# Kernel optimization log

Hardware: AMD Instinct MI355X
Metric: run time of the kernel (lower is better)

## Reference

```python
import jax, jax.numpy as jnp
import numpy as np

B = 8192      # batch size
D = 512       # feature dim == num_classes (centers is [C, C] in the original)
C = 512       # num_classes
MARGIN = 1.0


def setup_inputs() -> dict:
    key = jax.random.key(0)
    k1, k2, k3 = jax.random.split(key, 3)
    inputs = jax.random.normal(k1, (B, D), dtype=jnp.float32)
    targets = jax.random.randint(k2, (B,), 0, C)
    centers = jax.random.normal(k3, (C, D), dtype=jnp.float32)  # learned param
    return {"inputs": inputs, "targets": targets, "centers": centers}


def reference(inputs, targets, centers):
    # centers_batch[j] = centers[targets[j]]  (gather rows)
    cb = centers[targets]                                   # [B, D]
    # dist[i, j] = || inputs[i] - cb[j] ||_2, computed via the expanded form
    # (||a||^2 + ||b||^2 - 2 a.b) so we never materialize a [B, B, D] tensor.
    sq = ((inputs * inputs).sum(-1)[:, None]
          + (cb * cb).sum(-1)[None, :]
          - 2.0 * (inputs @ cb.T))                          # [B, B]
    dist = jnp.sqrt(jnp.clip(sq, 1e-12))                    # clamp(min=1e-12).sqrt()

    # mask[i, j] = (targets[i] == targets[j]); note original indexes dist[i][mask[i]]
    mask = targets[:, None] == targets[None, :]             # [B, B] bool
    dist_ap = jnp.max(jnp.where(mask, dist, -jnp.inf), axis=1)   # hardest positive per row
    dist_an = jnp.min(jnp.where(mask, jnp.inf, dist), axis=1)    # hardest negative per row

    # MarginRankingLoss(margin)(dist_an, dist_ap, y=1) = mean(relu(dist_ap - dist_an + margin))
    loss = jnp.mean(jnp.maximum(0.0, dist_ap - dist_an + MARGIN))
    prec = jnp.mean((dist_an > dist_ap).astype(jnp.float32))
    return loss, prec
```

## Files before the change

kernel.cpp:

```cpp
#include <hip/hip_runtime.h>
#include <hip/hip_bf16.h>

#define NB 8192
#define ND 512
#define NC 512
#define MARGIN_F 1.0f
#define BIGF 3.0e38f

typedef __attribute__((ext_vector_type(8))) short bf16x8;
typedef __attribute__((ext_vector_type(4))) float f32x4;

__device__ __forceinline__ unsigned fkey(float f) {
    unsigned u = __float_as_uint(f);
    unsigned mask = (u & 0x80000000u) ? 0xFFFFFFFFu : 0x80000000u;
    return u ^ mask;
}
__device__ __forceinline__ float finv(unsigned k) {
    unsigned mask = (k & 0x80000000u) ? 0x80000000u : 0xFFFFFFFFu;
    return __uint_as_float(k ^ mask);
}
__device__ __forceinline__ unsigned short f2bf(float f) {
    __hip_bfloat16 h = __float2bfloat16(f);
    return __builtin_bit_cast(unsigned short, h);
}

#define GLOAD_LDS16(g, l)                                                    \
    __builtin_amdgcn_global_load_lds(                                        \
        (const __attribute__((address_space(1))) void*)(g),                  \
        (__attribute__((address_space(3))) void*)(l), 16, 0, 0)

__global__ __launch_bounds__(256) void k0_prep(
    const float* __restrict__ inputs, const int* __restrict__ targets,
    const float* __restrict__ centers,
    unsigned short* __restrict__ inB, unsigned short* __restrict__ cenB,
    float* __restrict__ rsq, float* __restrict__ csq,
    unsigned* __restrict__ counts, unsigned* __restrict__ negmin)
{
    const int bid = blockIdx.x;
    const int tid = threadIdx.x;

    if (bid == 2176) {
        __shared__ unsigned hist[NC];
        for (int i = tid; i < NC; i += 256) hist[i] = 0u;
        __syncthreads();
        for (int i = tid; i < NB; i += 256) atomicAdd(&hist[targets[i]], 1u);
        __syncthreads();
        for (int i = tid; i < NC; i += 256) counts[i] = hist[i];
        return;
    }

    const int wave = tid >> 6, lane = tid & 63;
    const float* src;
    unsigned short* dst;
    float* sqdst;
    int row;
    bool is_input = (bid < 2048);
    if (is_input) {
        row   = bid * 4 + wave;
        src   = inputs + (size_t)row * ND;
        dst   = inB + (size_t)row * ND;
        sqdst = rsq + row;
    } else {
        row   = (bid - 2048) * 4 + wave;
        src   = centers + (size_t)row * ND;
        dst   = cenB + (size_t)row * ND;
        sqdst = csq + row;
    }

    float4 v1 = ((const float4*)src)[lane];
    float4 v2 = ((const float4*)src)[lane + 64];
    float s = v1.x*v1.x + v1.y*v1.y + v1.z*v1.z + v1.w*v1.w
            + v2.x*v2.x + v2.y*v2.y + v2.z*v2.z + v2.w*v2.w;

    ushort4 o1, o2;
    o1.x = f2bf(v1.x); o1.y = f2bf(v1.y); o1.z = f2bf(v1.z); o1.w = f2bf(v1.w);
    o2.x = f2bf(v2.x); o2.y = f2bf(v2.y); o2.z = f2bf(v2.z); o2.w = f2bf(v2.w);
    ((ushort4*)dst)[lane]      = o1;
    ((ushort4*)dst)[lane + 64] = o2;

    #pragma unroll
    for (int off = 32; off > 0; off >>= 1) s += __shfl_down(s, off);
    if (lane == 0) {
        *sqdst = s;
        if (is_input) negmin[row] = 0xFFFFFFFFu;
    }
}

__global__ __launch_bounds__(256) void k2_mfma(
    const unsigned short* __restrict__ Ain, const unsigned short* __restrict__ cenB,
    const int* __restrict__ targets, const unsigned* __restrict__ counts,
    const float* __restrict__ csq,
    unsigned* __restrict__ negmin, float* __restrict__ apval)
{
    __shared__ __align__(16) unsigned short As[16 * 512];
    __shared__ __align__(16) unsigned short Bs[8 * 512];
    __shared__ int      tgtL[128];
    __shared__ float    csqL[64];
    __shared__ unsigned ldsmin[128];

    const int tid  = threadIdx.x;
    const int w    = tid >> 6;
    const int lane = tid & 63;
    const int wm   = w >> 1;
    const int wn   = w & 1;
    const int ln   = lane & 15;
    const int kc8  = (lane >> 4) * 8;

    const int bid   = blockIdx.x;
    const int rbase = (bid & 63) * 128;
    const int cbase = (bid >> 6) * 64;

    if (tid < 128) { tgtL[tid] = targets[rbase + tid]; ldsmin[tid] = 0xFFFFFFFFu; }
    if (tid < 64) {
        const int c = cbase + tid;
        csqL[tid] = (counts[c] > 0u) ? csq[c] : BIGF;
    }

    const unsigned short* gAp[4];
    unsigned short*       lAp[4];
    #pragma unroll
    for (int t = 0; t < 4; ++t) {
        const int cid = 4 * w + t;
        const int rg = cid >> 1, kh = cid & 1;
        gAp[t] = Ain + (size_t)(rbase + rg * 16 + ln) * ND + kh * 32 + kc8;
        lAp[t] = &As[cid * 512];
    }
    const unsigned short* gBp[2];
    unsigned short*       lBp[2];
    #pragma unroll
    for (int t = 0; t < 2; ++t) {
        const int cid = 2 * w + t;
        gBp[t] = cenB + (size_t)(cbase + w * 16 + ln) * ND + t * 32 + kc8;
        lBp[t] = &Bs[cid * 512];
    }

    f32x4 acc[4][2] = {};

    for (int kb = 0; kb < ND; kb += 64) {
        __syncthreads();
        #pragma unroll
        for (int t = 0; t < 4; ++t) GLOAD_LDS16(gAp[t] + kb, lAp[t]);
        #pragma unroll
        for (int t = 0; t < 2; ++t) GLOAD_LDS16(gBp[t] + kb, lBp[t]);
        __syncthreads();

        #pragma unroll
        for (int ks = 0; ks < 2; ++ks) {
            bf16x8 a[4], b[2];
            #pragma unroll
            for (int i = 0; i < 4; ++i)
                a[i] = *(const bf16x8*)&As[((wm * 4 + i) * 2 + ks) * 512 + lane * 8];
            #pragma unroll
            for (int j = 0; j < 2; ++j)
                b[j] = *(const bf16x8*)&Bs[((wn * 2 + j) * 2 + ks) * 512 + lane * 8];
            #pragma unroll
            for (int i = 0; i < 4; ++i)
                #pragma unroll
                for (int j = 0; j < 2; ++j)
                    acc[i][j] = __builtin_amdgcn_mfma_f32_16x16x32_bf16(a[i], b[j], acc[i][j], 0, 0, 0);
        }
    }

    const int qd = lane >> 4;
    #pragma unroll
    for (int i = 0; i < 4; ++i) {
        #pragma unroll
        for (int r = 0; r < 4; ++r) {
            const int rlocal = wm * 64 + i * 16 + qd * 4 + r;
            const int grow   = rbase + rlocal;
            const int tr     = tgtL[rlocal];
            float m = BIGF;
            #pragma unroll
            for (int j = 0; j < 2; ++j) {
                const int clocal = wn * 32 + j * 16 + ln;
                const float val = csqL[clocal] - 2.0f * acc[i][j][r];
                if (cbase + clocal == tr) {
                    apval[grow] = val;
                } else {
                    m = fminf(m, val);
                }
            }
            #pragma unroll
            for (int off = 1; off < 16; off <<= 1)
                m = fminf(m, __shfl_xor(m, off));
            if (ln == 0) atomicMin(&ldsmin[rlocal], fkey(m));
        }
    }
    __syncthreads();
    if (tid < 128) {
        unsigned v = ldsmin[tid];
        if (v != 0xFFFFFFFFu) atomicMin(&negmin[rbase + tid], v);
    }
}

__global__ __launch_bounds__(1024) void k3_final(
    const float* __restrict__ rsq, const unsigned* __restrict__ negmin,
    const float* __restrict__ apval, float* __restrict__ out)
{
    __shared__ float sl[1024];
    __shared__ float sp[1024];
    const int tid = threadIdx.x;
    float a = 0.0f, p = 0.0f;
    for (int r = tid; r < NB; r += 1024) {
        float s  = rsq[r];
        float an = sqrtf(fmaxf(s + finv(negmin[r]), 1e-12f));
        float ap = sqrtf(fmaxf(s + apval[r], 1e-12f));
        a += fmaxf(0.0f, ap - an + MARGIN_F);
        p += (an > ap) ? 1.0f : 0.0f;
    }
    sl[tid] = a; sp[tid] = p;
    __syncthreads();
    #pragma unroll
    for (int s = 512; s > 0; s >>= 1) {
        if (tid < s) { sl[tid] += sl[tid + s]; sp[tid] += sp[tid + s]; }
        __syncthreads();
    }
    if (tid == 0) {
        out[0] = sl[0] / (float)NB;
        out[1] = sp[0] / (float)NB;
    }
}

extern "C" void kernel_launch(void* const* d_in, const int* in_sizes, int n_in,
                              void* d_out, int out_size, void* d_ws, size_t ws_size,
                              hipStream_t stream) {
    const float* inputs  = (const float*)d_in[0];
    const int*   targets = (const int*)d_in[1];
    const float* centers = (const float*)d_in[2];
    float* out = (float*)d_out;

    char* wp = (char*)d_ws;
    unsigned short* inB    = (unsigned short*)(wp);
    unsigned short* cenB   = (unsigned short*)(wp + 8388608);
    float*          rsq    = (float*)(wp + 8912896);
    float*          csqv   = (float*)(wp + 8945664);
    unsigned*       counts = (unsigned*)(wp + 8947712);
    unsigned*       negmin = (unsigned*)(wp + 8949760);
    float*          apval  = (float*)(wp + 8982528);

    k0_prep<<<2177, 256, 0, stream>>>(inputs, targets, centers,
                                      inB, cenB, rsq, csqv, counts, negmin);
    k2_mfma<<<512, 256, 0, stream>>>(inB, cenB, targets, counts, csqv,
                                     negmin, apval);
    k3_final<<<1, 1024, 0, stream>>>(rsq, negmin, apval, out);
}
```

Baseline: 97.63 us.

## Halve row tile to double grid and replace atomic min with per-tile partials

```diff
diff --git a/kernel.cpp b/kernel.cpp
--- a/kernel.cpp
+++ b/kernel.cpp
@@ -4,6 +4,7 @@
 #define NB 8192
 #define ND 512
 #define NC 512
+#define NCT 8
 #define MARGIN_F 1.0f
 #define BIGF 3.0e38f
 
@@ -34,7 +35,7 @@
     const float* __restrict__ centers,
     unsigned short* __restrict__ inB, unsigned short* __restrict__ cenB,
     float* __restrict__ rsq, float* __restrict__ csq,
-    unsigned* __restrict__ counts, unsigned* __restrict__ negmin)
+    unsigned* __restrict__ counts)
 {
     const int bid = blockIdx.x;
     const int tid = threadIdx.x;
@@ -80,23 +81,20 @@
 
     #pragma unroll
     for (int off = 32; off > 0; off >>= 1) s += __shfl_down(s, off);
-    if (lane == 0) {
-        *sqdst = s;
-        if (is_input) negmin[row] = 0xFFFFFFFFu;
-    }
+    if (lane == 0) *sqdst = s;
 }
 
 __global__ __launch_bounds__(256) void k2_mfma(
     const unsigned short* __restrict__ Ain, const unsigned short* __restrict__ cenB,
     const int* __restrict__ targets, const unsigned* __restrict__ counts,
     const float* __restrict__ csq,
-    unsigned* __restrict__ negmin, float* __restrict__ apval)
+    float* __restrict__ partmin, float* __restrict__ apval)
 {
-    __shared__ __align__(16) unsigned short As[16 * 512];
+    __shared__ __align__(16) unsigned short As[8 * 512];
     __shared__ __align__(16) unsigned short Bs[8 * 512];
-    __shared__ int      tgtL[128];
+    __shared__ int      tgtL[64];
     __shared__ float    csqL[64];
-    __shared__ unsigned ldsmin[128];
+    __shared__ unsigned ldsmin[64];
 
     const int tid  = threadIdx.x;
     const int w    = tid >> 6;
@@ -104,69 +102,65 @@
     const int wm   = w >> 1;
     const int wn   = w & 1;
     const int ln   = lane & 15;
-    const int kc8  = (lane >> 4) * 8;
+    const int qd   = lane >> 4;
 
     const int bid   = blockIdx.x;
-    const int rbase = (bid & 63) * 128;
-    const int cbase = (bid >> 6) * 64;
-
-    if (tid < 128) { tgtL[tid] = targets[rbase + tid]; ldsmin[tid] = 0xFFFFFFFFu; }
+    const int rbase = (bid & 127) * 64;
+    const int ct    = bid >> 7;
+    const int cbase = ct * 64;
+
     if (tid < 64) {
+        tgtL[tid]   = targets[rbase + tid];
         const int c = cbase + tid;
-        csqL[tid] = (counts[c] > 0u) ? csq[c] : BIGF;
-    }
-
-    const unsigned short* gAp[4];
-    unsigned short*       lAp[4];
-    #pragma unroll
-    for (int t = 0; t < 4; ++t) {
-        const int cid = 4 * w + t;
-        const int rg = cid >> 1, kh = cid & 1;
-        gAp[t] = Ain + (size_t)(rbase + rg * 16 + ln) * ND + kh * 32 + kc8;
-        lAp[t] = &As[cid * 512];
-    }
+        csqL[tid]   = (counts[c] > 0u) ? csq[c] : BIGF;
+        ldsmin[tid] = 0xFFFFFFFFu;
+    }
+
+    const unsigned short* gAp[2];
     const unsigned short* gBp[2];
-    unsigned short*       lBp[2];
+    unsigned short *lAp[2], *lBp[2];
     #pragma unroll
     for (int t = 0; t < 2; ++t) {
         const int cid = 2 * w + t;
-        gBp[t] = cenB + (size_t)(cbase + w * 16 + ln) * ND + t * 32 + kc8;
+        gAp[t] = Ain  + (size_t)(rbase + w * 16 + ln) * ND + t * 32 + qd * 8;
+        gBp[t] = cenB + (size_t)(cbase + w * 16 + ln) * ND + t * 32 + qd * 8;
+        lAp[t] = &As[cid * 512];
         lBp[t] = &Bs[cid * 512];
     }
 
-    f32x4 acc[4][2] = {};
+    f32x4 acc[2][2] = {};
 
     for (int kb = 0; kb < ND; kb += 64) {
         __syncthreads();
         #pragma unroll
-        for (int t = 0; t < 4; ++t) GLOAD_LDS16(gAp[t] + kb, lAp[t]);
-        #pragma unroll
-        for (int t = 0; t < 2; ++t) GLOAD_LDS16(gBp[t] + kb, lBp[t]);
+        for (int t = 0; t < 2; ++t) {
+            GLOAD_LDS16(gAp[t] + kb, lAp[t]);
+            GLOAD_LDS16(gBp[t] + kb, lBp[t]);
+        }
         __syncthreads();
 
         #pragma unroll
         for (int ks = 0; ks < 2; ++ks) {
-            bf16x8 a[4], b[2];
-            #pragma unroll
-            for (int i = 0; i < 4; ++i)
-                a[i] = *(const bf16x8*)&As[((wm * 4 + i) * 2 + ks) * 512 + lane * 8];
+            bf16x8 a[2], b[2];
+            #pragma unroll
+            for (int i = 0; i < 2; ++i)
+                a[i] = *(const bf16x8*)&As[((wm * 2 + i) * 2 + ks) * 512 + lane * 8];
             #pragma unroll
             for (int j = 0; j < 2; ++j)
                 b[j] = *(const bf16x8*)&Bs[((wn * 2 + j) * 2 + ks) * 512 + lane * 8];
             #pragma unroll
-            for (int i = 0; i < 4; ++i)
+            for (int i = 0; i < 2; ++i)
                 #pragma unroll
                 for (int j = 0; j < 2; ++j)
                     acc[i][j] = __builtin_amdgcn_mfma_f32_16x16x32_bf16(a[i], b[j], acc[i][j], 0, 0, 0);
         }
     }
 
-    const int qd = lane >> 4;
-    #pragma unroll
-    for (int i = 0; i < 4; ++i) {
+    #pragma unroll
+    for (int i = 0; i < 2; ++i) {
         #pragma unroll
         for (int r = 0; r < 4; ++r) {
-            const int rlocal = wm * 64 + i * 16 + qd * 4 + r;
+            const int rlocal = wm * 32 + i * 16 + qd * 4 + r;
             const int grow   = rbase + rlocal;
             const int tr     = tgtL[rlocal];
             float m = BIGF;
@@ -187,23 +181,27 @@
         }
     }
     __syncthreads();
-    if (tid < 128) {
-        unsigned v = ldsmin[tid];
-        if (v != 0xFFFFFFFFu) atomicMin(&negmin[rbase + tid], v);
-    }
+    if (tid < 64)
+        partmin[(size_t)(rbase + tid) * NCT + ct] = finv(ldsmin[tid]);
 }
 
 __global__ __launch_bounds__(1024) void k3_final(
-    const float* __restrict__ rsq, const unsigned* __restrict__ negmin,
+    const float* __restrict__ rsq, const float* __restrict__ partmin,
     const float* __restrict__ apval, float* __restrict__ out)
 {
     __shared__ float sl[1024];
     __shared__ float sp[1024];
     const int tid = threadIdx.x;
     float a = 0.0f, p = 0.0f;
-    for (int r = tid; r < NB; r += 1024) {
+    #pragma unroll
+    for (int it = 0; it < NB / 1024; ++it) {
+        const int r = it * 1024 + tid;
+        const float4* pm = (const float4*)&partmin[(size_t)r * NCT];
+        float4 m0 = pm[0], m1 = pm[1];
+        float m = fminf(fminf(fminf(m0.x, m0.y), fminf(m0.z, m0.w)),
+                        fminf(fminf(m1.x, m1.y), fminf(m1.z, m1.w)));
         float s  = rsq[r];
-        float an = sqrtf(fmaxf(s + finv(negmin[r]), 1e-12f));
+        float an = sqrtf(fmaxf(s + m,        1e-12f));
         float ap = sqrtf(fmaxf(s + apval[r], 1e-12f));
         a += fmaxf(0.0f, ap - an + MARGIN_F);
         p += (an > ap) ? 1.0f : 0.0f;
@@ -230,17 +228,17 @@
     float* out = (float*)d_out;
 
     char* wp = (char*)d_ws;
-    unsigned short* inB    = (unsigned short*)(wp);
-    unsigned short* cenB   = (unsigned short*)(wp + 8388608);
-    float*          rsq    = (float*)(wp + 8912896);
-    float*          csqv   = (float*)(wp + 8945664);
-    unsigned*       counts = (unsigned*)(wp + 8947712);
-    unsigned*       negmin = (unsigned*)(wp + 8949760);
-    float*          apval  = (float*)(wp + 8982528);
+    unsigned short* inB     = (unsigned short*)(wp);
+    unsigned short* cenB    = (unsigned short*)(wp + 8388608);
+    float*          rsq     = (float*)(wp + 8912896);
+    float*          csqv    = (float*)(wp + 8945664);
+    unsigned*       counts  = (unsigned*)(wp + 8947712);
+    float*          apval   = (float*)(wp + 8949760);
+    float*          partmin = (float*)(wp + 8982528);
 
     k0_prep<<<2177, 256, 0, stream>>>(inputs, targets, centers,
-                                      inB, cenB, rsq, csqv, counts, negmin);
-    k2_mfma<<<512, 256, 0, stream>>>(inB, cenB, targets, counts, csqv,
-                                     negmin, apval);
-    k3_final<<<1, 1024, 0, stream>>>(rsq, negmin, apval, out);
-}
+                                      inB, cenB, rsq, csqv, counts);
+    k2_mfma<<<1024, 256, 0, stream>>>(inB, cenB, targets, counts, csqv,
+                                      partmin, apval);
+    k3_final<<<1, 1024, 0, stream>>>(rsq, partmin, apval, out);
+}
```

Result: no change. 97.53 us (-0.1%).
